# Performance work log

Measured on AMD Instinct MI355X. Metric: run time of the kernel, lower is better.

Reference implementation:

```python
import jax, jax.numpy as jnp
import numpy as np

B, N, D = 4, 4096, 1024
H, DH = 16, 64  # heads, dim_head; inner_dim = H*DH = 1024
EPS = 1e-6


def setup_inputs() -> dict:
    key = jax.random.key(0)
    ks = jax.random.split(key, 6)
    s = 1.0 / np.sqrt(D)
    return {
        "x": jax.random.normal(ks[0], (B, N, D), dtype=jnp.float32),
        "Wq": jax.random.normal(ks[1], (D, H * DH), dtype=jnp.float32) * s,
        "Wk": jax.random.normal(ks[2], (D, H * DH), dtype=jnp.float32) * s,
        "Wv": jax.random.normal(ks[3], (D, H * DH), dtype=jnp.float32) * s,
        "Wo": jax.random.normal(ks[4], (H * DH, D), dtype=jnp.float32) * s,
        "bo": jnp.zeros((D,), dtype=jnp.float32),
    }


def reference(x, Wq, Wk, Wv, Wo, bo):
    # projections, split heads: b n (h d) -> b h n d
    def split_heads(t):
        b, n, _ = t.shape
        return t.reshape(b, n, H, DH).transpose(0, 2, 1, 3)

    q = split_heads(x @ Wq)
    k = split_heads(x @ Wk)  # context = x (self-attention)
    v = split_heads(x @ Wv)

    # elu feature map: elu(x) + 1
    q = jax.nn.elu(q) + 1.0
    k = jax.nn.elu(k) + 1.0

    # normalizer z[b,h,n,1] = q . sum_n k  + eps
    k_sum = k.sum(axis=2)                                  # b h d
    z = jnp.einsum('bhnd,bhd->bhn', q, k_sum)[..., None] + EPS

    # kv outer-product reduction: O(N d^2)
    kv = jnp.einsum('bhnd,bhne->bhde', k, v)               # b h d e
    out = jnp.einsum('bhnd,bhde->bhne', q, kv) / z         # b h n e

    # merge heads: b h n d -> b n (h d)
    out = out.transpose(0, 2, 1, 3).reshape(x.shape[0], x.shape[1], H * DH)
    return out @ Wo + bo
```

## Files before the change

kernel.cpp:

```cpp
#include <hip/hip_runtime.h>
#include <hip/hip_bf16.h>


#define DEV_INLINE __device__ __forceinline__

typedef short bf16x8 __attribute__((ext_vector_type(8)));
typedef float f32x4  __attribute__((ext_vector_type(4)));

static constexpr int Bb = 4, Nn = 4096, Dd = 1024, Hh = 16, DHd = 64;
static constexpr int Mrows = Bb * Nn;

DEV_INLINE float bf2f(short s) {
  unsigned u = ((unsigned)(unsigned short)s) << 16;
  float f; __builtin_memcpy(&f, &u, 4); return f;
}
DEV_INLINE short f2bf(float f) {
  unsigned u; __builtin_memcpy(&u, &f, 4);
  unsigned r = (u + 0x7fffu + ((u >> 16) & 1u)) >> 16;
  return (short)r;
}

DEV_INLINE void gload16(const void* g, void* l) {
  typedef __attribute__((address_space(1))) const void gv_t;
  typedef __attribute__((address_space(3))) void lv_t;
  __builtin_amdgcn_global_load_lds((gv_t*)g, (lv_t*)l, 16, 0, 0);
}

DEV_INLINE int lds_off(int r_, int c_) {
  return r_ * 128 + ((((c_ >> 3) ^ (r_ & 7)) << 3) | (c_ & 7));
}


__global__ void convert_x_kernel(const float* __restrict__ x, short* __restrict__ xb) {
  const int total = Mrows * 1024 / 4;
  for (int i = blockIdx.x * 256 + threadIdx.x; i < total; i += 2048 * 256) {
    float4 v = ((const float4*)x)[i];
    short4 o;
    o.x = f2bf(v.x); o.y = f2bf(v.y); o.z = f2bf(v.z); o.w = f2bf(v.w);
    ((short4*)xb)[i] = o;
  }
}

__global__ void transposeW_kernel(const float* __restrict__ Wq, const float* __restrict__ Wk,
                                  const float* __restrict__ Wv, const float* __restrict__ Wo,
                                  short* __restrict__ Wt, short* __restrict__ WoT,
                                  float* __restrict__ ksum) {
  int z = blockIdx.z;
  int t = threadIdx.x;
  if (z == 0 && blockIdx.y == 0 && blockIdx.x < 16)
    ksum[blockIdx.x * 256 + t] = 0.f;
  const float* W = (z == 0) ? Wq : (z == 1) ? Wk : (z == 2) ? Wv : Wo;
  short* dstb = (z < 3) ? (Wt + (size_t)z * 1024 * 1024) : WoT;
  __shared__ float tile[64][69];
  int r = t >> 2, c4 = (t & 3) << 4;
  const float* src = W + (blockIdx.y * 64 + r) * 1024 + blockIdx.x * 64 + c4;
  for (int j = 0; j < 4; ++j) {
    float4 v = ((const float4*)src)[j];
    tile[r][c4 + 4 * j + 0] = v.x;
    tile[r][c4 + 4 * j + 1] = v.y;
    tile[r][c4 + 4 * j + 2] = v.z;
    tile[r][c4 + 4 * j + 3] = v.w;
  }
  __syncthreads();
  __attribute__((aligned(16))) short tmp[16];
  for (int j = 0; j < 16; ++j) tmp[j] = f2bf(tile[c4 + j][r]);
  short* dst = dstb + (blockIdx.x * 64 + r) * 1024 + blockIdx.y * 64 + c4;
  ((int4*)dst)[0] = ((int4*)tmp)[0];
  ((int4*)dst)[1] = ((int4*)tmp)[1];
}

template <int MODE>
__global__ __launch_bounds__(256, 4) void gemm128_kernel(
    const short* __restrict__ A, const short* __restrict__ Bt,
    short* __restrict__ q, short* __restrict__ kT, short* __restrict__ vT,
    float* __restrict__ out, const float* __restrict__ bias,
    float* __restrict__ ksum, int nTilesN) {
  __shared__ __align__(16) short sm[128 * 128];
  short* smA = sm;
  short* smB = sm + 8192;
  const int K = 1024;
  int bid0 = blockIdx.x;
  int xcd = bid0 & 7, local = bid0 >> 3;
  int chunk = local >> 6, rem = local & 63;
  int ncc = nTilesN >> 3;
  int cm = chunk / ncc, cn = chunk % ncc;
  int tm = xcd * 16 + cm * 8 + (rem >> 3);
  int tn = cn * 8 + (rem & 7);

  int t = threadIdx.x, w = t >> 6, lane = t & 63;
  int rl = lane & 15, kg = lane >> 4;
  int wr = w >> 1, wc = w & 1;
  const short* Abase = A + (size_t)tm * 128 * K;
  const short* Bbase = Bt + (size_t)tn * 128 * K;

  f32x4 acc[4][4] = {};
  for (int k0 = 0; k0 < K; k0 += 64) {
    __syncthreads();
    for (int p = 0; p < 4; ++p) {
      int c = p * 256 + t;
      int row = c >> 3, u = c & 7;
      int off = ((u ^ (row & 7)) << 3);
      gload16(Abase + row * K + k0 + off, (char*)smA + p * 4096 + w * 1024);
      gload16(Bbase + row * K + k0 + off, (char*)smB + p * 4096 + w * 1024);
    }
    __syncthreads();
    for (int kk = 0; kk < 2; ++kk) {
      int slot = kk * 4 + kg;
      bf16x8 af[4], bfr[4];
      for (int mt = 0; mt < 4; ++mt) {
        int row = wr * 64 + mt * 16 + rl;
        af[mt] = *(const bf16x8*)&smA[row * 64 + ((slot ^ (row & 7)) << 3)];
      }
      for (int nt = 0; nt < 4; ++nt) {
        int row = wc * 64 + nt * 16 + rl;
        bfr[nt] = *(const bf16x8*)&smB[row * 64 + ((slot ^ (row & 7)) << 3)];
      }
      for (int mt = 0; mt < 4; ++mt)
        for (int nt = 0; nt < 4; ++nt)
          acc[mt][nt] = __builtin_amdgcn_mfma_f32_16x16x32_bf16(af[mt], bfr[nt], acc[mt][nt], 0, 0, 0);
    }
  }
  if (MODE == 1) {
    float* smf = (float*)sm;
    __syncthreads();
    for (int h = 0; h < 2; ++h) {
      if (wr == h) {
        for (int mt = 0; mt < 4; ++mt)
          for (int nt = 0; nt < 4; ++nt)
            for (int r = 0; r < 4; ++r)
              smf[(mt * 16 + kg * 4 + r) * 128 + wc * 64 + nt * 16 + rl] = acc[mt][nt][r];
      }
      __syncthreads();
      for (int i = 0; i < 8; ++i) {
        int idx = i * 256 + t;
        int row = idx >> 5, c4 = (idx & 31) << 2;
        float4 v = *(const float4*)&smf[row * 128 + c4];
        float4 bv = *(const float4*)&bias[tn * 128 + c4];
        v.x += bv.x; v.y += bv.y; v.z += bv.z; v.w += bv.w;
        *(float4*)&out[(size_t)(tm * 128 + h * 64 + row) * Dd + tn * 128 + c4] = v;
      }
      __syncthreads();
    }
    return;
  }
  __syncthreads();
  int sec = tn >> 3;
  int tloc = tn & 7;
  for (int mt = 0; mt < 4; ++mt)
    for (int nt = 0; nt < 4; ++nt)
      for (int r = 0; r < 4; ++r) {
        float v = acc[mt][nt][r];
        if (sec <= 1) v = v > 0.f ? v + 1.f : __expf(v);
        int row = wr * 64 + mt * 16 + kg * 4 + r;
        int col = wc * 64 + nt * 16 + rl;
        int o = (sec == 0) ? lds_off(row, col) : lds_off(col, row);
        sm[o] = f2bf(v);
      }
  __syncthreads();
  if (sec == 0) {
    for (int i = 0; i < 8; ++i) {
      int idx = i * 256 + t;
      int row = idx >> 4, c = idx & 15;
      int col0 = c * 8;
      int gcol = tloc * 128 + col0;
      int h = gcol >> 6, d0 = gcol & 63;
      int grow = tm * 128 + row;
      int b = grow >> 12, n = grow & 4095;
      *(int4*)&q[(((size_t)(b * Hh + h)) * Nn + n) * DHd + d0] = *(const int4*)&sm[lds_off(row, col0)];
    }
  } else {
    short* dst = (sec == 1) ? kT : vT;
    for (int i = 0; i < 8; ++i) {
      int idx = i * 256 + t;
      int dcol = idx >> 4, c = idx & 15;
      int n0 = c * 8;
      int gcol = tloc * 128 + dcol;
      int h = gcol >> 6, d = gcol & 63;
      int grow0 = tm * 128 + n0;
      int b = grow0 >> 12, n = grow0 & 4095;
      *(int4*)&dst[(((size_t)(b * Hh + h)) * DHd + d) * Nn + n] = *(const int4*)&sm[lds_off(dcol, n0)];
    }
    if (sec == 1) {
      int dcol = t >> 1, half = t & 1;
      float s = 0.f;
      for (int c = half * 64; c < half * 64 + 64; ++c)
        s += bf2f(sm[lds_off(dcol, c)]);
      s += __shfl_xor(s, 1);
      if (half == 0) {
        int g = tloc * 128 + dcol;
        int h = g >> 6, d = g & 63;
        int b = (tm * 128) >> 12;
        atomicAdd(&ksum[(b * Hh + h) * DHd + d], s);
      }
    }
  }
}

__global__ __launch_bounds__(256, 2) void kv_kernel(const short* __restrict__ kT,
                                                    const short* __restrict__ vT,
                                                    float* __restrict__ kvp) {
  __shared__ __align__(16) short smK[64 * 128];
  __shared__ __align__(16) short smV[64 * 128];
  int bh = blockIdx.x, seg = blockIdx.y;
  int t = threadIdx.x;
  int w = t >> 6, lane = t & 63, rl = lane & 15, kg = lane >> 4;
  const short* kb = kT + (size_t)bh * DHd * Nn + seg * 512;
  const short* vb = vT + (size_t)bh * DHd * Nn + seg * 512;
  f32x4 acc[4] = {};
  for (int n0 = 0; n0 < 512; n0 += 128) {
    __syncthreads();
    for (int p = 0; p < 4; ++p) {
      int c = p * 256 + t;
      int row = c >> 4, u = c & 15;
      int off = ((u ^ (row & 15)) << 3);
      gload16(kb + row * Nn + n0 + off, (char*)smK + p * 4096 + w * 1024);
      gload16(vb + row * Nn + n0 + off, (char*)smV + p * 4096 + w * 1024);
    }
    __syncthreads();
    for (int kk = 0; kk < 4; ++kk) {
      int slot = kk * 4 + kg;
      int rowA = w * 16 + rl;
      bf16x8 a = *(const bf16x8*)&smK[rowA * 128 + ((slot ^ (rowA & 15)) << 3)];
      for (int nt = 0; nt < 4; ++nt) {
        int rowB = nt * 16 + rl;
        bf16x8 b = *(const bf16x8*)&smV[rowB * 128 + ((slot ^ (rowB & 15)) << 3)];
        acc[nt] = __builtin_amdgcn_mfma_f32_16x16x32_bf16(a, b, acc[nt], 0, 0, 0);
      }
    }
  }
  float* smf = (float*)smK;
  __syncthreads();
  for (int nt = 0; nt < 4; ++nt)
    for (int r = 0; r < 4; ++r)
      smf[(nt * 16 + rl) * 64 + (w * 16 + kg * 4 + r)] = acc[nt][r];
  __syncthreads();
  float* dst = kvp + ((size_t)(bh * 8 + seg)) * 4096;
  for (int i = 0; i < 4; ++i) {
    int idx = i * 256 + t;
    int e = idx >> 4, c4 = (idx & 15) << 2;
    *(float4*)&dst[e * 64 + c4] = *(const float4*)&smf[e * 64 + c4];
  }
}

__global__ void kvc_kernel(const float* __restrict__ kvp, short* __restrict__ kvT) {
  int bh = blockIdx.x, t = threadIdx.x;
  const float* p0 = kvp + (size_t)bh * 8 * 4096;
  for (int rep = 0; rep < 4; ++rep) {
    int idx = rep * 1024 + t * 4;
    float4 s = *(const float4*)&p0[idx];
    for (int j = 1; j < 8; ++j) {
      float4 a = *(const float4*)&p0[j * 4096 + idx];
      s.x += a.x; s.y += a.y; s.z += a.z; s.w += a.w;
    }
    short4 o;
    o.x = f2bf(s.x); o.y = f2bf(s.y); o.z = f2bf(s.z); o.w = f2bf(s.w);
    *(short4*)&kvT[(size_t)bh * 4096 + idx] = o;
  }
}

__global__ __launch_bounds__(256, 2) void attn_kernel(const short* __restrict__ q,
                                                      const short* __restrict__ kvT,
                                                      const float* __restrict__ ksum,
                                                      short* __restrict__ attn) {
  int rb = blockIdx.x, bh = blockIdx.y;
  int b = bh >> 4, h = bh & 15;
  __shared__ float sks[64];
  __shared__ __align__(16) short satt[64 * 64];
  int t = threadIdx.x, w = t >> 6, lane = t & 63, rl = lane & 15, kg = lane >> 4;
  if (t < 64) sks[t] = ksum[bh * 64 + t];
  __syncthreads();
  int row0 = rb * 64 + w * 16;
  const short* qb = q + ((size_t)bh * Nn + row0) * DHd;
  const short* kvb = kvT + (size_t)bh * 4096;
  f32x4 acc[4] = {};
  float zp = 0.f;
  for (int kk = 0; kk < 2; ++kk) {
    int kb = kk * 32 + kg * 8;
    bf16x8 a = *(const bf16x8*)&qb[rl * DHd + kb];
    for (int j = 0; j < 8; ++j) zp += bf2f(a[j]) * sks[kb + j];
    for (int nt = 0; nt < 4; ++nt) {
      bf16x8 bfr = *(const bf16x8*)&kvb[(nt * 16 + rl) * 64 + kb];
      acc[nt] = __builtin_amdgcn_mfma_f32_16x16x32_bf16(a, bfr, acc[nt], 0, 0, 0);
    }
  }
  zp += __shfl_xor(zp, 16);
  zp += __shfl_xor(zp, 32);
  float zr[4];
  for (int r = 0; r < 4; ++r) zr[r] = __shfl(zp, kg * 4 + r);
  for (int nt = 0; nt < 4; ++nt)
    for (int r = 0; r < 4; ++r)
      satt[(w * 16 + kg * 4 + r) * 64 + nt * 16 + rl] = f2bf(acc[nt][r] / (zr[r] + 1e-6f));
  __syncthreads();
  for (int i = 0; i < 2; ++i) {
    int idx = i * 256 + t;
    int row = idx >> 3, c8 = (idx & 7) << 3;
    int n = rb * 64 + row;
    *(int4*)&attn[((size_t)(b * Nn + n)) * 1024 + h * 64 + c8] = *(const int4*)&satt[row * 64 + c8];
  }
}

extern "C" void kernel_launch(void* const* d_in, const int* in_sizes, int n_in,
                              void* d_out, int out_size, void* d_ws, size_t ws_size,
                              hipStream_t stream) {
  const float* x  = (const float*)d_in[0];
  const float* Wq = (const float*)d_in[1];
  const float* Wk = (const float*)d_in[2];
  const float* Wv = (const float*)d_in[3];
  const float* Wo = (const float*)d_in[4];
  const float* bo = (const float*)d_in[5];
  float* out = (float*)d_out;

  char* ws = (char*)d_ws;
  size_t off = 0;
  auto alloc = [&](size_t bytes) {
    char* p = ws + off;
    off += (bytes + 255) & ~(size_t)255;
    return p;
  };
  short* xb   = (short*)alloc((size_t)Mrows * 1024 * 2);
  short* Wt   = (short*)alloc((size_t)3072 * 1024 * 2);
  short* WoT  = (short*)alloc((size_t)1024 * 1024 * 2);
  short* qb   = (short*)alloc((size_t)64 * Nn * DHd * 2);
  short* kT   = (short*)alloc((size_t)64 * DHd * Nn * 2);
  short* vT   = (short*)alloc((size_t)64 * DHd * Nn * 2);
  float* ksum = (float*)alloc((size_t)64 * 64 * 4);
  float* kvp  = (float*)alloc((size_t)64 * 8 * 4096 * 4);
  short* kvT  = (short*)alloc((size_t)64 * 4096 * 2);
  short* attn = (short*)alloc((size_t)Mrows * 1024 * 2);

  convert_x_kernel<<<2048, 256, 0, stream>>>(x, xb);
  transposeW_kernel<<<dim3(16, 16, 4), 256, 0, stream>>>(Wq, Wk, Wv, Wo, Wt, WoT, ksum);

  gemm128_kernel<0><<<3072, 256, 0, stream>>>(xb, Wt, qb, kT, vT, nullptr, nullptr, ksum, 24);
  kv_kernel<<<dim3(64, 8), 256, 0, stream>>>(kT, vT, kvp);
  kvc_kernel<<<64, 256, 0, stream>>>(kvp, kvT);
  attn_kernel<<<dim3(64, 64), 256, 0, stream>>>(qb, kvT, ksum, attn);
  gemm128_kernel<1><<<1024, 256, 0, stream>>>(attn, WoT, nullptr, nullptr, nullptr, out, bo, nullptr, 8);
}
```

Before: 235.1 us.

## Use 32x32 MFMA in GEMMs, merge prep kernels, split KV reduction finer

```diff
diff --git a/kernel.cpp b/kernel.cpp
--- a/kernel.cpp
+++ b/kernel.cpp
@@ -6,6 +6,7 @@
 
 typedef short bf16x8 __attribute__((ext_vector_type(8)));
 typedef float f32x4  __attribute__((ext_vector_type(4)));
+typedef float f32x16 __attribute__((ext_vector_type(16)));
 
 static constexpr int Bb = 4, Nn = 4096, Dd = 1024, Hh = 16, DHd = 64;
 static constexpr int Mrows = Bb * Nn;
@@ -30,24 +31,26 @@
   return r_ * 128 + ((((c_ >> 3) ^ (r_ & 7)) << 3) | (c_ & 7));
 }
 
-
-__global__ void convert_x_kernel(const float* __restrict__ x, short* __restrict__ xb) {
-  const int total = Mrows * 1024 / 4;
-  for (int i = blockIdx.x * 256 + threadIdx.x; i < total; i += 2048 * 256) {
-    float4 v = ((const float4*)x)[i];
-    short4 o;
-    o.x = f2bf(v.x); o.y = f2bf(v.y); o.z = f2bf(v.z); o.w = f2bf(v.w);
-    ((short4*)xb)[i] = o;
-  }
-}
-
-__global__ void transposeW_kernel(const float* __restrict__ Wq, const float* __restrict__ Wk,
-                                  const float* __restrict__ Wv, const float* __restrict__ Wo,
-                                  short* __restrict__ Wt, short* __restrict__ WoT,
-                                  float* __restrict__ ksum) {
+__global__ void prep_kernel(const float* __restrict__ x,
+                            const float* __restrict__ Wq, const float* __restrict__ Wk,
+                            const float* __restrict__ Wv, const float* __restrict__ Wo,
+                            short* __restrict__ xb, short* __restrict__ Wt,
+                            short* __restrict__ WoT, float* __restrict__ ksum) {
   int z = blockIdx.z;
   int t = threadIdx.x;
-  if (z == 0 && blockIdx.y == 0 && blockIdx.x < 16)
+  if (z == 4) {
+    int bid = blockIdx.y * 64 + blockIdx.x;
+    const int total = Mrows * 1024 / 4;
+    for (int i = bid * 256 + t; i < total; i += 1024 * 256) {
+      float4 v = ((const float4*)x)[i];
+      short4 o;
+      o.x = f2bf(v.x); o.y = f2bf(v.y); o.z = f2bf(v.z); o.w = f2bf(v.w);
+      ((short4*)xb)[i] = o;
+    }
+    return;
+  }
+  if (blockIdx.x >= 16) return;
+  if (z == 0 && blockIdx.y == 0)
     ksum[blockIdx.x * 256 + t] = 0.f;
   const float* W = (z == 0) ? Wq : (z == 1) ? Wk : (z == 2) ? Wv : Wo;
   short* dstb = (z < 3) ? (Wt + (size_t)z * 1024 * 1024) : WoT;
@@ -70,7 +73,7 @@
 }
 
 template <int MODE>
-__global__ __launch_bounds__(256, 4) void gemm128_kernel(
+__global__ __launch_bounds__(256, 3) void gemm128_kernel(
     const short* __restrict__ A, const short* __restrict__ Bt,
     short* __restrict__ q, short* __restrict__ kT, short* __restrict__ vT,
     float* __restrict__ out, const float* __restrict__ bias,
@@ -88,12 +91,15 @@
   int tn = cn * 8 + (rem & 7);
 
   int t = threadIdx.x, w = t >> 6, lane = t & 63;
-  int rl = lane & 15, kg = lane >> 4;
+  int rl31 = lane & 31, hi = lane >> 5;
   int wr = w >> 1, wc = w & 1;
   const short* Abase = A + (size_t)tm * 128 * K;
   const short* Bbase = Bt + (size_t)tn * 128 * K;
 
-  f32x4 acc[4][4] = {};
+  f32x16 acc[2][2] = {};
+  const int rA0 = wr * 64 + rl31, rA1 = rA0 + 32;
+  const int rB0 = wc * 64 + rl31, rB1 = rB0 + 32;
+
   for (int k0 = 0; k0 < K; k0 += 64) {
     __syncthreads();
     for (int p = 0; p < 4; ++p) {
@@ -104,31 +110,35 @@
       gload16(Bbase + row * K + k0 + off, (char*)smB + p * 4096 + w * 1024);
     }
     __syncthreads();
-    for (int kk = 0; kk < 2; ++kk) {
-      int slot = kk * 4 + kg;
-      bf16x8 af[4], bfr[4];
-      for (int mt = 0; mt < 4; ++mt) {
-        int row = wr * 64 + mt * 16 + rl;
-        af[mt] = *(const bf16x8*)&smA[row * 64 + ((slot ^ (row & 7)) << 3)];
-      }
-      for (int nt = 0; nt < 4; ++nt) {
-        int row = wc * 64 + nt * 16 + rl;
-        bfr[nt] = *(const bf16x8*)&smB[row * 64 + ((slot ^ (row & 7)) << 3)];
-      }
-      for (int mt = 0; mt < 4; ++mt)
-        for (int nt = 0; nt < 4; ++nt)
-          acc[mt][nt] = __builtin_amdgcn_mfma_f32_16x16x32_bf16(af[mt], bfr[nt], acc[mt][nt], 0, 0, 0);
-    }
-  }
+#pragma unroll
+    for (int ks = 0; ks < 4; ++ks) {
+      int sl = ks * 2 + hi;
+      bf16x8 a0 = *(const bf16x8*)&smA[rA0 * 64 + ((sl ^ (rA0 & 7)) << 3)];
+      bf16x8 a1 = *(const bf16x8*)&smA[rA1 * 64 + ((sl ^ (rA1 & 7)) << 3)];
+      bf16x8 b0 = *(const bf16x8*)&smB[rB0 * 64 + ((sl ^ (rB0 & 7)) << 3)];
+      bf16x8 b1 = *(const bf16x8*)&smB[rB1 * 64 + ((sl ^ (rB1 & 7)) << 3)];
+      acc[0][0] = __builtin_amdgcn_mfma_f32_32x32x16_bf16(a0, b0, acc[0][0], 0, 0, 0);
+      acc[0][1] = __builtin_amdgcn_mfma_f32_32x32x16_bf16(a0, b1, acc[0][1], 0, 0, 0);
+      acc[1][0] = __builtin_amdgcn_mfma_f32_32x32x16_bf16(a1, b0, acc[1][0], 0, 0, 0);
+      acc[1][1] = __builtin_amdgcn_mfma_f32_32x32x16_bf16(a1, b1, acc[1][1], 0, 0, 0);
+    }
+  }
+
   if (MODE == 1) {
     float* smf = (float*)sm;
     __syncthreads();
     for (int h = 0; h < 2; ++h) {
       if (wr == h) {
-        for (int mt = 0; mt < 4; ++mt)
-          for (int nt = 0; nt < 4; ++nt)
-            for (int r = 0; r < 4; ++r)
-              smf[(mt * 16 + kg * 4 + r) * 128 + wc * 64 + nt * 16 + rl] = acc[mt][nt][r];
+#pragma unroll
+        for (int mt = 0; mt < 2; ++mt)
+#pragma unroll
+          for (int nt = 0; nt < 2; ++nt)
+#pragma unroll
+            for (int r = 0; r < 16; ++r) {
+              int lrow = mt * 32 + (r & 3) + 8 * (r >> 2) + 4 * hi;
+              int col = wc * 64 + nt * 32 + rl31;
+              smf[lrow * 128 + col] = acc[mt][nt][r];
+            }
       }
       __syncthreads();
       for (int i = 0; i < 8; ++i) {
@@ -146,13 +156,16 @@
   __syncthreads();
   int sec = tn >> 3;
   int tloc = tn & 7;
-  for (int mt = 0; mt < 4; ++mt)
-    for (int nt = 0; nt < 4; ++nt)
-      for (int r = 0; r < 4; ++r) {
+#pragma unroll
+  for (int mt = 0; mt < 2; ++mt)
+#pragma unroll
+    for (int nt = 0; nt < 2; ++nt)
+#pragma unroll
+      for (int r = 0; r < 16; ++r) {
         float v = acc[mt][nt][r];
         if (sec <= 1) v = v > 0.f ? v + 1.f : __expf(v);
-        int row = wr * 64 + mt * 16 + kg * 4 + r;
-        int col = wc * 64 + nt * 16 + rl;
+        int row = wr * 64 + mt * 32 + (r & 3) + 8 * (r >> 2) + 4 * hi;
+        int col = wc * 64 + nt * 32 + rl31;
         int o = (sec == 0) ? lds_off(row, col) : lds_off(col, row);
         sm[o] = f2bf(v);
       }
@@ -204,10 +217,10 @@
   int bh = blockIdx.x, seg = blockIdx.y;
   int t = threadIdx.x;
   int w = t >> 6, lane = t & 63, rl = lane & 15, kg = lane >> 4;
-  const short* kb = kT + (size_t)bh * DHd * Nn + seg * 512;
-  const short* vb = vT + (size_t)bh * DHd * Nn + seg * 512;
+  const short* kb = kT + (size_t)bh * DHd * Nn + seg * 256;
+  const short* vb = vT + (size_t)bh * DHd * Nn + seg * 256;
   f32x4 acc[4] = {};
-  for (int n0 = 0; n0 < 512; n0 += 128) {
+  for (int n0 = 0; n0 < 256; n0 += 128) {
     __syncthreads();
     for (int p = 0; p < 4; ++p) {
       int c = p * 256 + t;
@@ -220,11 +233,11 @@
     for (int kk = 0; kk < 4; ++kk) {
       int slot = kk * 4 + kg;
       int rowA = w * 16 + rl;
-      bf16x8 a = *(const bf16x8*)&smK[rowA * 128 + ((slot ^ (rowA & 15)) << 3)];
+      bf16x8 av = *(const bf16x8*)&smK[rowA * 128 + ((slot ^ (rowA & 15)) << 3)];
       for (int nt = 0; nt < 4; ++nt) {
         int rowB = nt * 16 + rl;
-        bf16x8 b = *(const bf16x8*)&smV[rowB * 128 + ((slot ^ (rowB & 15)) << 3)];
-        acc[nt] = __builtin_amdgcn_mfma_f32_16x16x32_bf16(a, b, acc[nt], 0, 0, 0);
+        bf16x8 bv = *(const bf16x8*)&smV[rowB * 128 + ((slot ^ (rowB & 15)) << 3)];
+        acc[nt] = __builtin_amdgcn_mfma_f32_16x16x32_bf16(av, bv, acc[nt], 0, 0, 0);
       }
     }
   }
@@ -234,7 +247,7 @@
     for (int r = 0; r < 4; ++r)
       smf[(nt * 16 + rl) * 64 + (w * 16 + kg * 4 + r)] = acc[nt][r];
   __syncthreads();
-  float* dst = kvp + ((size_t)(bh * 8 + seg)) * 4096;
+  float* dst = kvp + ((size_t)(bh * 16 + seg)) * 4096;
   for (int i = 0; i < 4; ++i) {
     int idx = i * 256 + t;
     int e = idx >> 4, c4 = (idx & 15) << 2;
@@ -244,13 +257,14 @@
 
 __global__ void kvc_kernel(const float* __restrict__ kvp, short* __restrict__ kvT) {
   int bh = blockIdx.x, t = threadIdx.x;
-  const float* p0 = kvp + (size_t)bh * 8 * 4096;
+  const float* p0 = kvp + (size_t)bh * 16 * 4096;
   for (int rep = 0; rep < 4; ++rep) {
     int idx = rep * 1024 + t * 4;
     float4 s = *(const float4*)&p0[idx];
-    for (int j = 1; j < 8; ++j) {
-      float4 a = *(const float4*)&p0[j * 4096 + idx];
-      s.x += a.x; s.y += a.y; s.z += a.z; s.w += a.w;
+#pragma unroll
+    for (int j = 1; j < 16; ++j) {
+      float4 aa = *(const float4*)&p0[(size_t)j * 4096 + idx];
+      s.x += aa.x; s.y += aa.y; s.z += aa.z; s.w += aa.w;
     }
     short4 o;
     o.x = f2bf(s.x); o.y = f2bf(s.y); o.z = f2bf(s.z); o.w = f2bf(s.w);
@@ -276,11 +290,11 @@
   float zp = 0.f;
   for (int kk = 0; kk < 2; ++kk) {
     int kb = kk * 32 + kg * 8;
-    bf16x8 a = *(const bf16x8*)&qb[rl * DHd + kb];
-    for (int j = 0; j < 8; ++j) zp += bf2f(a[j]) * sks[kb + j];
+    bf16x8 av = *(const bf16x8*)&qb[rl * DHd + kb];
+    for (int j = 0; j < 8; ++j) zp += bf2f(av[j]) * sks[kb + j];
     for (int nt = 0; nt < 4; ++nt) {
       bf16x8 bfr = *(const bf16x8*)&kvb[(nt * 16 + rl) * 64 + kb];
-      acc[nt] = __builtin_amdgcn_mfma_f32_16x16x32_bf16(a, bfr, acc[nt], 0, 0, 0);
+      acc[nt] = __builtin_amdgcn_mfma_f32_16x16x32_bf16(av, bfr, acc[nt], 0, 0, 0);
     }
   }
   zp += __shfl_xor(zp, 16);
@@ -324,15 +338,14 @@
   short* kT   = (short*)alloc((size_t)64 * DHd * Nn * 2);
   short* vT   = (short*)alloc((size_t)64 * DHd * Nn * 2);
   float* ksum = (float*)alloc((size_t)64 * 64 * 4);
-  float* kvp  = (float*)alloc((size_t)64 * 8 * 4096 * 4);
+  float* kvp  = (float*)alloc((size_t)64 * 16 * 4096 * 4);
   short* kvT  = (short*)alloc((size_t)64 * 4096 * 2);
   short* attn = (short*)alloc((size_t)Mrows * 1024 * 2);
 
-  convert_x_kernel<<<2048, 256, 0, stream>>>(x, xb);
-  transposeW_kernel<<<dim3(16, 16, 4), 256, 0, stream>>>(Wq, Wk, Wv, Wo, Wt, WoT, ksum);
+  prep_kernel<<<dim3(64, 16, 5), 256, 0, stream>>>(x, Wq, Wk, Wv, Wo, xb, Wt, WoT, ksum);
 
   gemm128_kernel<0><<<3072, 256, 0, stream>>>(xb, Wt, qb, kT, vT, nullptr, nullptr, ksum, 24);
-  kv_kernel<<<dim3(64, 8), 256, 0, stream>>>(kT, vT, kvp);
+  kv_kernel<<<dim3(64, 16), 256, 0, stream>>>(kT, vT, kvp);
   kvc_kernel<<<64, 256, 0, stream>>>(kvp, kvT);
   attn_kernel<<<dim3(64, 64), 256, 0, stream>>>(qb, kvT, ksum, attn);
   gemm128_kernel<1><<<1024, 256, 0, stream>>>(attn, WoT, nullptr, nullptr, nullptr, out, bo, nullptr, 8);
```

After: 263.0 us. +11.9%, slower.
